# Kernel optimization log

Measured on AMD Instinct MI355X. Metric: run time of the kernel, lower is better.

## Reference

```python
import jax, jax.numpy as jnp
import numpy as np

INPUT_DIM = 1024
NUM_HEADS = 16
HEAD_DIM = INPUT_DIM // NUM_HEADS


def setup_inputs() -> dict:
    key = jax.random.key(0)
    ks = jax.random.split(key, 9)
    d = INPUT_DIM
    s = 1.0 / np.sqrt(d)
    x = jax.random.normal(ks[0], (2, 2048, d), dtype=jnp.float32)
    # nn.Linear default init ~ U(-1/sqrt(in), 1/sqrt(in)); weights stored as (out, in), we keep (in, out)
    Wq = jax.random.uniform(ks[1], (d, d), jnp.float32, -s, s)
    bq = jax.random.uniform(ks[2], (d,), jnp.float32, -s, s)
    Wk = jax.random.uniform(ks[3], (d, d), jnp.float32, -s, s)
    bk = jax.random.uniform(ks[4], (d,), jnp.float32, -s, s)
    Wv = jax.random.uniform(ks[5], (d, d), jnp.float32, -s, s)
    bv = jax.random.uniform(ks[6], (d,), jnp.float32, -s, s)
    Wo = jax.random.uniform(ks[7], (d, d), jnp.float32, -s, s)
    bo = jax.random.uniform(ks[8], (d,), jnp.float32, -s, s)
    return {"x": x, "Wq": Wq, "bq": bq, "Wk": Wk, "bk": bk, "Wv": Wv, "bv": bv, "Wo": Wo, "bo": bo}


def reference(x, Wq, bq, Wk, bk, Wv, bv, Wo, bo):
    b, t, d = x.shape
    h, hd = NUM_HEADS, HEAD_DIM
    # projections -> [b, h, t, hd]
    q = (x @ Wq + bq).reshape(b, t, h, hd).transpose(0, 2, 1, 3)
    k = (x @ Wk + bk).reshape(b, t, h, hd).transpose(0, 2, 1, 3)
    v = (x @ Wv + bv).reshape(b, t, h, hd).transpose(0, 2, 1, 3)
    scores = jnp.einsum('bhqd,bhkd->bhqk', q, k) / jnp.sqrt(jnp.float32(hd))
    probs = jax.nn.softmax(scores, axis=-1)
    out = jnp.einsum('bhqk,bhkd->bhqd', probs, v)
    out = out.transpose(0, 2, 1, 3).reshape(b, t, d)
    return out @ Wo + bo
```

## Files before the change

### kernel.cpp

```cpp
#include <hip/hip_runtime.h>
#include <math.h>


#define BATCH 2
#define SEQ   2048
#define DIM   1024
#define NHEAD 16
#define HDIM  64
#define MROWS (BATCH * SEQ)
#define BH    (BATCH * NHEAD)
#define NKT   (SEQ / 64)

typedef __attribute__((ext_vector_type(4))) float     floatx4;
typedef __attribute__((ext_vector_type(4))) float     float4v;
typedef __attribute__((ext_vector_type(8))) _Float16  half8;
typedef __attribute__((ext_vector_type(4))) _Float16  half4;
typedef __attribute__((ext_vector_type(2))) __fp16    fp16x2;
typedef __attribute__((ext_vector_type(4))) unsigned  uint4v;

#define SOFT_C 5.77078016f
#define QSCALE 0.18033688f

#if __has_builtin(__builtin_amdgcn_exp2f)
#define EXP2F(x) __builtin_amdgcn_exp2f(x)
#else
#define EXP2F(x) exp2f(x)
#endif

__device__ __forceinline__ void gload16(const void* g, void* l) {
    __builtin_amdgcn_global_load_lds(
        (const __attribute__((address_space(1))) unsigned int*)g,
        (__attribute__((address_space(3))) unsigned int*)l, 16, 0, 0);
}

__device__ __forceinline__ unsigned pk2(float a, float b) {
    fp16x2 v = __builtin_amdgcn_cvt_pkrtz(a, b);
    return __builtin_bit_cast(unsigned, v);
}

__device__ __forceinline__ void plswap(unsigned &a, unsigned &b) {
#if __has_builtin(__builtin_amdgcn_permlane32_swap) && __has_builtin(__builtin_amdgcn_permlane16_swap)
    auto r32 = __builtin_amdgcn_permlane32_swap(a, b, false, false);
    auto r16 = __builtin_amdgcn_permlane16_swap(r32[0], r32[1], false, false);
    a = r16[0]; b = r16[1];
#else
    asm volatile("s_nop 1\n\t"
                 "v_permlane32_swap_b32 %0, %1\n\t"
                 "s_nop 1\n\t"
                 "v_permlane16_swap_b32 %0, %1\n\t"
                 "s_nop 1"
                 : "+v"(a), "+v"(b));
#endif
}

__global__ __launch_bounds__(256) void prep(
    const float* __restrict__ x,
    const float* __restrict__ Wq, const float* __restrict__ Wk,
    const float* __restrict__ Wv, const float* __restrict__ Wo,
    _Float16* __restrict__ xh,
    _Float16* __restrict__ Wqt, _Float16* __restrict__ Wkt,
    _Float16* __restrict__ Wvt, _Float16* __restrict__ Wot)
{
    const int tid = threadIdx.x;
    if (blockIdx.z == 4) {
        const int bid = blockIdx.y * 16 + blockIdx.x;
        #pragma unroll
        for (int it = 0; it < 8; ++it) {
            const size_t i = (((size_t)it * 256 + bid) * 256 + tid) * 8;
            float4v a = *(const float4v*)(x + i);
            float4v b = *(const float4v*)(x + i + 4);
            half8 o;
            #pragma unroll
            for (int c = 0; c < 4; ++c) { o[c] = (_Float16)a[c]; o[4+c] = (_Float16)b[c]; }
            *(half8*)(xh + i) = o;
        }
        return;
    }
    __shared__ float tile[64][65];
    const float* W; _Float16* o;
    switch (blockIdx.z) {
        case 0: W = Wq; o = Wqt; break;
        case 1: W = Wk; o = Wkt; break;
        case 2: W = Wv; o = Wvt; break;
        default: W = Wo; o = Wot; break;
    }
    const int n0 = blockIdx.x * 64, k0 = blockIdx.y * 64;
    #pragma unroll
    for (int p = 0; p < 16; ++p) {
        int idx = tid + p * 256;
        int r = idx >> 6, c = idx & 63;
        tile[r][c] = W[(size_t)(k0 + r) * DIM + n0 + c];
    }
    __syncthreads();
    #pragma unroll
    for (int p = 0; p < 16; ++p) {
        int idx = tid + p * 256;
        int r = idx >> 6, c = idx & 63;
        o[(size_t)(n0 + r) * DIM + k0 + c] = (_Float16)tile[c][r];
    }
}

__device__ __forceinline__ void gemm_core32(
    const _Float16* __restrict__ Ap, const _Float16* __restrict__ Bp,
    int m0, int n0, _Float16* SH, floatx4 acc[4][4])
{
    const int tid  = threadIdx.x;
    const int wave = tid >> 6;
    const int lane = tid & 63;
    const int li   = lane & 15;
    const int quad = lane >> 4;
    const int wm   = (wave >> 1) * 64;
    const int wn   = (wave & 1) * 64;

    _Float16* AL0 = SH;
    _Float16* BL0 = SH + 4096;
    _Float16* AL1 = SH + 8192;
    _Float16* BL1 = SH + 12288;

    auto stg = [&](int k0, _Float16* AL, _Float16* BL) {
        #pragma unroll
        for (int p = 0; p < 2; ++p) {
            int s = tid + p * 256;
            int r = s >> 2, ks = s & 3;
            int kg = (ks ^ ((r >> 1) & 3)) << 3;
            int ldsb = (wave * 64 + p * 256) * 8;
            gload16(Ap + (size_t)(m0 + r) * DIM + k0 + kg, AL + ldsb);
            gload16(Bp + (size_t)(n0 + r) * DIM + k0 + kg, BL + ldsb);
        }
    };

    auto cmp = [&](const _Float16* AL, const _Float16* BL) {
        half8 a[4], b[4];
        const int cs = (quad ^ ((li >> 1) & 3)) << 3;
        #pragma unroll
        for (int i = 0; i < 4; ++i) {
            a[i] = *(const half8*)(AL + ((wm + i * 16 + li) << 5) + cs);
            b[i] = *(const half8*)(BL + ((wn + i * 16 + li) << 5) + cs);
        }
        #pragma unroll
        for (int i = 0; i < 4; ++i)
            #pragma unroll
            for (int j = 0; j < 4; ++j)
                acc[i][j] = __builtin_amdgcn_mfma_f32_16x16x32_f16(a[i], b[j], acc[i][j], 0, 0, 0);
    };

    stg(0, AL0, BL0);
    __syncthreads();

    for (int kt = 0; kt < DIM / 32; kt += 2) {
        stg((kt + 1) * 32, AL1, BL1);
        __builtin_amdgcn_s_setprio(1);
        cmp(AL0, BL0);
        __builtin_amdgcn_s_setprio(0);
        __syncthreads();
        if (kt + 2 < DIM / 32) stg((kt + 2) * 32, AL0, BL0);
        __builtin_amdgcn_s_setprio(1);
        cmp(AL1, BL1);
        __builtin_amdgcn_s_setprio(0);
        __syncthreads();
    }
}

__global__ __launch_bounds__(256, 2) void qkv_mfma(
    const _Float16* __restrict__ xh,
    const _Float16* __restrict__ Wqt, const _Float16* __restrict__ Wkt,
    const _Float16* __restrict__ Wvt,
    const float* __restrict__ bq, const float* __restrict__ bk,
    const float* __restrict__ bv,
    _Float16* __restrict__ Qh, _Float16* __restrict__ Kh,
    _Float16* __restrict__ Vth)
{
    __shared__ __align__(16) _Float16 SH[128 * 128];

    const int bid = blockIdx.x + 8 * (blockIdx.y + 32 * blockIdx.z);
    const int swz = (bid & 7) * 96 + (bid >> 3);
    const int bx  = swz & 7;
    const int by  = (swz >> 3) & 31;
    const int z   = swz >> 8;

    const _Float16* Bp; const float* bias;
    if (z == 0)      { Bp = Wqt; bias = bq; }
    else if (z == 1) { Bp = Wkt; bias = bk; }
    else             { Bp = Wvt; bias = bv; }

    const int m0 = by * 128, n0 = bx * 128;

    floatx4 acc[4][4];
    #pragma unroll
    for (int i = 0; i < 4; ++i)
        #pragma unroll
        for (int j = 0; j < 4; ++j) acc[i][j] = (floatx4){0.f, 0.f, 0.f, 0.f};

    gemm_core32(xh, Bp, m0, n0, SH, acc);

    const int tid = threadIdx.x, wave = tid >> 6, lane = tid & 63;
    const int li = lane & 15, quad = lane >> 4;
    const int wm = (wave >> 1) * 64, wn = (wave & 1) * 64;
    const int bb = m0 >> 11, t0 = m0 & 2047;

    if (z != 2) {
        _Float16* out = (z == 0) ? Qh : Kh;
        const float sc = (z == 0) ? QSCALE : 1.0f;
        #pragma unroll
        for (int i = 0; i < 4; ++i)
            #pragma unroll
            for (int j = 0; j < 4; ++j) {
                int n = n0 + wn + j * 16 + li;
                int h = n >> 6, hd = n & 63;
                float b_ = bias[n];
                #pragma unroll
                for (int r = 0; r < 4; ++r) {
                    int m = m0 + wm + i * 16 + quad * 4 + r;
                    int t = m & 2047;
                    out[(((size_t)(bb * NHEAD + h) * SEQ) + t) * HDIM + hd] =
                        (_Float16)((acc[i][j][r] + b_) * sc);
                }
            }
    } else {
        __syncthreads();
        #pragma unroll
        for (int i = 0; i < 4; ++i)
            #pragma unroll
            for (int j = 0; j < 4; ++j) {
                int n = wn + j * 16 + li;
                float b_ = bias[n0 + n];
                half4 w;
                #pragma unroll
                for (int r = 0; r < 4; ++r) w[r] = (_Float16)(acc[i][j][r] + b_);
                int col  = wm + i * 16 + quad * 4;
                int colp = ((((col >> 3) ^ (n & 7)) << 3)) | (col & 7);
                *(half4*)(SH + n * 128 + colp) = w;
            }
        __syncthreads();
        #pragma unroll
        for (int p = 0; p < 8; ++p) {
            int idx = p * 256 + tid;
            int v = idx >> 4, c8 = (idx & 15) * 8;
            int c8p = (((c8 >> 3) ^ (v & 7)) << 3);
            half8 w = *(const half8*)(SH + v * 128 + c8p);
            int n = n0 + v;
            int h = n >> 6, hd = n & 63;
            *(half8*)(Vth + ((size_t)(bb * NHEAD + h) * HDIM + hd) * SEQ + t0 + c8) = w;
        }
    }
}

__global__ __launch_bounds__(256, 2) void attn(
    const _Float16* __restrict__ Q, const _Float16* __restrict__ K,
    const _Float16* __restrict__ Vt,
    _Float16* __restrict__ Ctx)
{
    __shared__ __align__(16) _Float16 Ks[2][64 * 64];
    __shared__ __align__(16) _Float16 Vs[2][64 * 64];

    const int tid  = threadIdx.x;
    const int wave = tid >> 6;
    const int lane = tid & 63;
    const int li   = lane & 15;
    const int quad = lane >> 4;

    const int bid = blockIdx.x + 16 * blockIdx.y;
    const int swz = (bid & 7) * 64 + (bid >> 3);
    const int q0  = (swz & 15) * 128;
    const int bh  = swz >> 4;
    const int b   = bh >> 4, h = bh & 15;

    half8 qa[2][2];
    #pragma unroll
    for (int nq = 0; nq < 2; ++nq) {
        size_t qrow = ((size_t)bh * SEQ + q0 + wave * 32 + nq * 16 + li) * HDIM;
        qa[nq][0] = *(const half8*)(Q + qrow + quad * 8);
        qa[nq][1] = *(const half8*)(Q + qrow + 32 + quad * 8);
    }

    half8 onesA;
    {
        _Float16 v = (li == 0) ? (_Float16)1.0f : (_Float16)0.0f;
        #pragma unroll
        for (int c = 0; c < 8; ++c) onesA[c] = v;
    }

    floatx4 O[4][2];
    floatx4 rsacc[2];
    #pragma unroll
    for (int nq = 0; nq < 2; ++nq) {
        rsacc[nq] = (floatx4){0.f, 0.f, 0.f, 0.f};
        #pragma unroll
        for (int i = 0; i < 4; ++i) O[i][nq] = (floatx4){0.f, 0.f, 0.f, 0.f};
    }

    const _Float16* Kbh = K  + (size_t)bh * SEQ * HDIM;
    const _Float16* Vbh = Vt + (size_t)bh * HDIM * SEQ;

    auto stage = [&](int buf, int kt_) {
        const _Float16* Kg = Kbh + (size_t)kt_ * 64 * HDIM;
        const _Float16* Vg = Vbh + kt_ * 64;
        _Float16* Kl = &Ks[buf][0];
        _Float16* Vl = &Vs[buf][0];
        #pragma unroll
        for (int p = 0; p < 2; ++p) {
            int s = tid + p * 256;
            int r = s >> 3, ks = s & 7;
            int kg = (ks ^ (r & 7)) << 3;
            int ldsb = (wave * 64 + p * 256) * 8;
            gload16(Kg + r * HDIM + kg, Kl + ldsb);
            gload16(Vg + (size_t)r * SEQ + kg, Vl + ldsb);
        }
    };

    auto qk_phase = [&](const _Float16* Kc, const _Float16* Vc,
                        half8 (&pbN)[2][2], half8 (&vfN)[4][2]) {
        unsigned R[2][4][2];
        #pragma unroll
        for (int mb = 0; mb < 4; ++mb) {
            int row = (mb * 16 + li) << 6;
            half8 a0 = *(const half8*)(Kc + row + ((quad ^ (li & 7)) << 3));
            half8 a1 = *(const half8*)(Kc + row + (((quad + 4) ^ (li & 7)) << 3));
            #pragma unroll
            for (int nq = 0; nq < 2; ++nq) {
                floatx4 st = (floatx4){-SOFT_C, -SOFT_C, -SOFT_C, -SOFT_C};
                st = __builtin_amdgcn_mfma_f32_16x16x32_f16(a0, qa[nq][0], st, 0, 0, 0);
                st = __builtin_amdgcn_mfma_f32_16x16x32_f16(a1, qa[nq][1], st, 0, 0, 0);
                R[nq][mb][0] = pk2(EXP2F(st[0]), EXP2F(st[1]));
                R[nq][mb][1] = pk2(EXP2F(st[2]), EXP2F(st[3]));
            }
        }
        #pragma unroll
        for (int nq = 0; nq < 2; ++nq)
            #pragma unroll
            for (int f = 0; f < 2; ++f) {
                unsigned w0, w1, w2, w3;
                {
                    unsigned x = R[nq][2 * f][0], y = R[nq][2 * f + 1][0];
                    plswap(x, y);
                    w0 = x; w2 = y;
                }
                {
                    unsigned x = R[nq][2 * f][1], y = R[nq][2 * f + 1][1];
                    plswap(x, y);
                    w1 = x; w3 = y;
                }
                uint4v uw; uw[0] = w0; uw[1] = w1; uw[2] = w2; uw[3] = w3;
                pbN[nq][f] = __builtin_bit_cast(half8, uw);
            }
        #pragma unroll
        for (int mb = 0; mb < 4; ++mb) {
            int row = (mb * 16 + li) << 6;
            vfN[mb][0] = *(const half8*)(Vc + row + ((quad ^ (li & 7)) << 3));
            vfN[mb][1] = *(const half8*)(Vc + row + (((quad + 4) ^ (li & 7)) << 3));
        }
    };

    auto pv_phase = [&](half8 (&pbP)[2][2], half8 (&vfP)[4][2]) {
        #pragma unroll
        for (int nq = 0; nq < 2; ++nq) {
            rsacc[nq] = __builtin_amdgcn_mfma_f32_16x16x32_f16(onesA, pbP[nq][0], rsacc[nq], 0, 0, 0);
            rsacc[nq] = __builtin_amdgcn_mfma_f32_16x16x32_f16(onesA, pbP[nq][1], rsacc[nq], 0, 0, 0);
        }
        #pragma unroll
        for (int mb = 0; mb < 4; ++mb)
            #pragma unroll
            for (int nq = 0; nq < 2; ++nq) {
                O[mb][nq] = __builtin_amdgcn_mfma_f32_16x16x32_f16(vfP[mb][0], pbP[nq][0], O[mb][nq], 0, 0, 0);
                O[mb][nq] = __builtin_amdgcn_mfma_f32_16x16x32_f16(vfP[mb][1], pbP[nq][1], O[mb][nq], 0, 0, 0);
            }
    };

    half8 pbA[2][2], pbB[2][2];
    half8 vfA[4][2], vfB[4][2];

    stage(0, 0);
    __syncthreads();

    stage(1, 1);
    __builtin_amdgcn_s_setprio(1);
    qk_phase(&Ks[0][0], &Vs[0][0], pbA, vfA);
    __builtin_amdgcn_s_setprio(0);
    __syncthreads();

    for (int kt = 1; kt < NKT - 1; kt += 2) {
        stage(0, kt + 1);
        __builtin_amdgcn_s_setprio(1);
        pv_phase(pbA, vfA);
        qk_phase(&Ks[1][0], &Vs[1][0], pbB, vfB);
        __builtin_amdgcn_s_setprio(0);
        __syncthreads();

        stage(1, kt + 2);
        __builtin_amdgcn_s_setprio(1);
        pv_phase(pbB, vfB);
        qk_phase(&Ks[0][0], &Vs[0][0], pbA, vfA);
        __builtin_amdgcn_s_setprio(0);
        __syncthreads();
    }

    __builtin_amdgcn_s_setprio(1);
    pv_phase(pbA, vfA);
    qk_phase(&Ks[1][0], &Vs[1][0], pbB, vfB);
    pv_phase(pbB, vfB);
    __builtin_amdgcn_s_setprio(0);
    __syncthreads();

    float inv[2];
    #pragma unroll
    for (int nq = 0; nq < 2; ++nq) {
        float rs = __shfl(rsacc[nq][0], li, 64);
        inv[nq] = 1.0f / rs;
    }

    _Float16* Sw = &Ks[0][0] + wave * (32 * 64);
    #pragma unroll
    for (int mb = 0; mb < 4; ++mb)
        #pragma unroll
        for (int nq = 0; nq < 2; ++nq) {
            uint2 w;
            w.x = pk2(O[mb][nq][0] * inv[nq], O[mb][nq][1] * inv[nq]);
            w.y = pk2(O[mb][nq][2] * inv[nq], O[mb][nq][3] * inv[nq]);
            int row = nq * 16 + li;
            int col = mb * 16 + quad * 4;
            int swc = (((col >> 3) ^ (row & 7)) << 3) | (col & 7);
            *(uint2*)(Sw + row * 64 + swc) = w;
        }
    __builtin_amdgcn_s_waitcnt(0);
    #pragma unroll
    for (int p = 0; p < 4; ++p) {
        int idx = p * 64 + lane;
        int qq = idx >> 3, c = idx & 7;
        half8 v = *(const half8*)(Sw + qq * 64 + ((c ^ (qq & 7)) << 3));
        size_t row = (size_t)b * SEQ + q0 + wave * 32 + qq;
        *(half8*)(Ctx + row * DIM + h * HDIM + c * 8) = v;
    }
}

__global__ __launch_bounds__(256, 2) void out_mfma(
    const _Float16* __restrict__ Ctx, const _Float16* __restrict__ Wot,
    const float* __restrict__ bo, float* __restrict__ out)
{
    __shared__ __align__(16) _Float16 SH[4 * 4096];

    const int bid = blockIdx.x + 8 * blockIdx.y;
    const int swz = (bid & 7) * 32 + (bid >> 3);
    const int m0 = (swz >> 3) * 128, n0 = (swz & 7) * 128;

    floatx4 acc[4][4];
    #pragma unroll
    for (int i = 0; i < 4; ++i)
        #pragma unroll
        for (int j = 0; j < 4; ++j) acc[i][j] = (floatx4){0.f, 0.f, 0.f, 0.f};

    gemm_core32(Ctx, Wot, m0, n0, SH, acc);

    const int tid = threadIdx.x, wave = tid >> 6, lane = tid & 63;
    const int li = lane & 15, quad = lane >> 4;
    const int wm = (wave >> 1) * 64, wn = (wave & 1) * 64;

    #pragma unroll
    for (int i = 0; i < 4; ++i)
        #pragma unroll
        for (int j = 0; j < 4; ++j) {
            int n = n0 + wn + j * 16 + li;
            float b_ = bo[n];
            #pragma unroll
            for (int r = 0; r < 4; ++r) {
                int m = m0 + wm + i * 16 + quad * 4 + r;
                out[(size_t)m * DIM + n] = acc[i][j][r] + b_;
            }
        }
}

extern "C" void kernel_launch(void* const* d_in, const int* in_sizes, int n_in,
                              void* d_out, int out_size, void* d_ws, size_t ws_size,
                              hipStream_t stream) {
    const float* x  = (const float*)d_in[0];
    const float* Wq = (const float*)d_in[1];
    const float* bq = (const float*)d_in[2];
    const float* Wk = (const float*)d_in[3];
    const float* bk = (const float*)d_in[4];
    const float* Wv = (const float*)d_in[5];
    const float* bv = (const float*)d_in[6];
    const float* Wo = (const float*)d_in[7];
    const float* bo = (const float*)d_in[8];
    float* out = (float*)d_out;

    const size_t PX = (size_t)MROWS * DIM;
    const size_t PW = (size_t)DIM * DIM;
    _Float16* xh  = (_Float16*)d_ws;
    _Float16* Wqt = xh + PX;
    _Float16* Wkt = Wqt + PW;
    _Float16* Wvt = Wkt + PW;
    _Float16* Wot = Wvt + PW;
    _Float16* Qh  = Wot + PW;
    _Float16* Kh  = Qh + PX;
    _Float16* spare = Kh + PX;
    _Float16* Vth = spare + PX;

    _Float16* Ctx = xh;

    prep<<<dim3(16, 16, 5), 256, 0, stream>>>(
        x, Wq, Wk, Wv, Wo, xh, Wqt, Wkt, Wvt, Wot);

    qkv_mfma<<<dim3(DIM / 128, MROWS / 128, 3), 256, 0, stream>>>(
        xh, Wqt, Wkt, Wvt, bq, bk, bv, Qh, Kh, Vth);

    attn<<<dim3(SEQ / 128, BH), 256, 0, stream>>>(
        Qh, Kh, Vth, Ctx);

    out_mfma<<<dim3(DIM / 128, MROWS / 128), 256, 0, stream>>>(
        Ctx, Wot, bo, out);
}
```

Before: 178.1 us.

## Retile output projection GEMM to 64x128 tiles with K=64 stages

The output projection kernel drops the shared gemm_core32 and gets its own loop with 64x128 output tiles and 64-wide K stages, double-buffered in LDS. This doubles the block count to 512 so more of the CUs have work, and halves the number of K iterations and barriers. Both GEMM kernels also raise launch_bounds minimum blocks per CU from 2 to 3 to push occupancy, at the risk of the register cap causing spills or worse scheduling. The smaller M tile lowers per-block reuse of the weight matrix.

```diff
diff --git a/kernel.cpp b/kernel.cpp
--- a/kernel.cpp
+++ b/kernel.cpp
@@ -161,7 +161,7 @@
     }
 }
 
-__global__ __launch_bounds__(256, 2) void qkv_mfma(
+__global__ __launch_bounds__(256, 3) void qkv_mfma(
     const _Float16* __restrict__ xh,
     const _Float16* __restrict__ Wqt, const _Float16* __restrict__ Wkt,
     const _Float16* __restrict__ Wvt,
@@ -432,30 +432,97 @@
     }
 }
 
-__global__ __launch_bounds__(256, 2) void out_mfma(
+__global__ __launch_bounds__(256, 3) void out_mfma(
     const _Float16* __restrict__ Ctx, const _Float16* __restrict__ Wot,
     const float* __restrict__ bo, float* __restrict__ out)
 {
-    __shared__ __align__(16) _Float16 SH[4 * 4096];
+    __shared__ __align__(16) _Float16 SH[24576];
 
     const int bid = blockIdx.x + 8 * blockIdx.y;
-    const int swz = (bid & 7) * 32 + (bid >> 3);
-    const int m0 = (swz >> 3) * 128, n0 = (swz & 7) * 128;
-
-    floatx4 acc[4][4];
-    #pragma unroll
-    for (int i = 0; i < 4; ++i)
+    const int swz = (bid & 7) * 64 + (bid >> 3);
+    const int bx = swz & 7, by = swz >> 3;
+    const int m0 = by * 64, n0 = bx * 128;
+
+    const int tid  = threadIdx.x;
+    const int wave = tid >> 6;
+    const int lane = tid & 63;
+    const int li   = lane & 15;
+    const int quad = lane >> 4;
+    const int wm   = (wave >> 1) * 32;
+    const int wn   = (wave & 1) * 64;
+
+    _Float16* A0 = SH;
+    _Float16* B0 = SH + 4096;
+    _Float16* A1 = SH + 12288;
+    _Float16* B1 = SH + 16384;
+
+    floatx4 acc[2][4];
+    #pragma unroll
+    for (int i = 0; i < 2; ++i)
         #pragma unroll
         for (int j = 0; j < 4; ++j) acc[i][j] = (floatx4){0.f, 0.f, 0.f, 0.f};
 
-    gemm_core32(Ctx, Wot, m0, n0, SH, acc);
-
-    const int tid = threadIdx.x, wave = tid >> 6, lane = tid & 63;
-    const int li = lane & 15, quad = lane >> 4;
-    const int wm = (wave >> 1) * 64, wn = (wave & 1) * 64;
-
-    #pragma unroll
-    for (int i = 0; i < 4; ++i)
+    auto stg = [&](int k0, _Float16* AL, _Float16* BL) {
+        #pragma unroll
+        for (int p = 0; p < 2; ++p) {
+            int s = tid + p * 256;
+            int r = s >> 3, ks = s & 7;
+            int kg = (ks ^ (r & 7)) << 3;
+            gload16(Ctx + (size_t)(m0 + r) * DIM + k0 + kg,
+                    AL + (wave * 64 + p * 256) * 8);
+        }
+        #pragma unroll
+        for (int p = 0; p < 4; ++p) {
+            int s = tid + p * 256;
+            int r = s >> 3, ks = s & 7;
+            int kg = (ks ^ (r & 7)) << 3;
+            gload16(Wot + (size_t)(n0 + r) * DIM + k0 + kg,
+                    BL + (wave * 64 + p * 256) * 8);
+        }
+    };
+
+    auto cmp = [&](const _Float16* AL, const _Float16* BL) {
+        half8 a[2][2], b[4][2];
+        #pragma unroll
+        for (int i = 0; i < 2; ++i) {
+            int ra = (wm + i * 16 + li) << 6;
+            #pragma unroll
+            for (int hh = 0; hh < 2; ++hh)
+                a[i][hh] = *(const half8*)(AL + ra + (((hh * 4 + quad) ^ (li & 7)) << 3));
+        }
+        #pragma unroll
+        for (int j = 0; j < 4; ++j) {
+            int rb = (wn + j * 16 + li) << 6;
+            #pragma unroll
+            for (int hh = 0; hh < 2; ++hh)
+                b[j][hh] = *(const half8*)(BL + rb + (((hh * 4 + quad) ^ (li & 7)) << 3));
+        }
+        #pragma unroll
+        for (int i = 0; i < 2; ++i)
+            #pragma unroll
+            for (int j = 0; j < 4; ++j) {
+                acc[i][j] = __builtin_amdgcn_mfma_f32_16x16x32_f16(a[i][0], b[j][0], acc[i][j], 0, 0, 0);
+                acc[i][j] = __builtin_amdgcn_mfma_f32_16x16x32_f16(a[i][1], b[j][1], acc[i][j], 0, 0, 0);
+            }
+    };
+
+    stg(0, A0, B0);
+    __syncthreads();
+    for (int kt = 0; kt < DIM / 64; kt += 2) {
+        stg((kt + 1) * 64, A1, B1);
+        __builtin_amdgcn_s_setprio(1);
+        cmp(A0, B0);
+        __builtin_amdgcn_s_setprio(0);
+        __syncthreads();
+        if (kt + 2 < DIM / 64) stg((kt + 2) * 64, A0, B0);
+        __builtin_amdgcn_s_setprio(1);
+        cmp(A1, B1);
+        __builtin_amdgcn_s_setprio(0);
+        __syncthreads();
+    }
+
+    #pragma unroll
+    for (int i = 0; i < 2; ++i)
         #pragma unroll
         for (int j = 0; j < 4; ++j) {
             int n = n0 + wn + j * 16 + li;
@@ -505,6 +572,6 @@
     attn<<<dim3(SEQ / 128, BH), 256, 0, stream>>>(
         Qh, Kh, Vth, Ctx);
 
-    out_mfma<<<dim3(DIM / 128, MROWS / 128), 256, 0, stream>>>(
+    out_mfma<<<dim3(8, MROWS / 64), 256, 0, stream>>>(
         Ctx, Wot, bo, out);
 }
```

After: 176.7 us. About the same (-0.8%).
